# Kernel tuning notes

Hardware: AMD Instinct MI355X
Metric: run time of the kernel (lower is better)

The kernel has to match this reference:

```python
import jax, jax.numpy as jnp
import numpy as np

N_NODES = 20000
N_EDGES = 320000
N_GRAPHS = 64
SEQ = 20
SCALAR = 16
EMB = 32
HID = 128
HEADS = 4
IN_DIM = SCALAR + 5 * EMB  # 176
NEG_SLOPE = 0.2


def masked_mean_embed(table, idx):
    # table: [V, EMB], idx: [N, L] with 0 = padding
    emb = table[idx]                                  # [N, L, EMB]
    mask = (idx != 0).astype(emb.dtype)[..., None]    # [N, L, 1]
    return (emb * mask).sum(axis=1) / (mask.sum(axis=1) + 1e-9)


def gat_conv(x, src, dst, W, att_src, att_dst, bias, heads, out_ch):
    # PyG GATConv (add_self_loops already applied to src/dst), concat heads.
    N = x.shape[0]
    xw = (x @ W).reshape(N, heads, out_ch)            # [N, H, C]
    a_src = (xw * att_src).sum(-1)                    # [N, H]
    a_dst = (xw * att_dst).sum(-1)                    # [N, H]
    e = jax.nn.leaky_relu(a_src[src] + a_dst[dst], NEG_SLOPE)  # [E, H]
    e_max = jax.ops.segment_max(e, dst, num_segments=N)
    e_max = jnp.where(jnp.isfinite(e_max), e_max, 0.0)
    ex = jnp.exp(e - e_max[dst])                      # [E, H]
    denom = jax.ops.segment_sum(ex, dst, num_segments=N)
    alpha = ex / (denom[dst] + 1e-16)                 # [E, H]
    msg = xw[src] * alpha[:, :, None]                 # [E, H, C]
    out = jax.ops.segment_sum(msg, dst, num_segments=N)
    return out.reshape(N, heads * out_ch) + bias


def setup_inputs() -> dict:
    key = jax.random.key(0)
    ks = jax.random.split(key, 24)
    s = 0.05
    inp = {
        "x_scalar": jax.random.normal(ks[0], (N_NODES, SCALAR), jnp.float32),
        "x_opcode": jax.random.randint(ks[1], (N_NODES, SEQ), 0, 256),
        "x_source": jax.random.randint(ks[2], (N_NODES, SEQ), 0, 512),
        "x_sink": jax.random.randint(ks[3], (N_NODES, SEQ), 0, 512),
        "x_string_manip": jax.random.randint(ks[4], (N_NODES, SEQ), 0, 128),
        "x_payload": jax.random.randint(ks[5], (N_NODES, SEQ), 0, 1024),
        "edge_index": jax.random.randint(ks[6], (2, N_EDGES), 0, N_NODES),
        "batch": jnp.sort(jax.random.randint(ks[7], (N_NODES,), 0, N_GRAPHS)),
        # embedding tables (row 0 = padding; masked out anyway)
        "emb_opcode": jax.random.normal(ks[8], (256, EMB)) * s,
        "emb_source": jax.random.normal(ks[9], (512, EMB)) * s,
        "emb_sink": jax.random.normal(ks[10], (512, EMB)) * s,
        "emb_string": jax.random.normal(ks[11], (128, EMB)) * s,
        "emb_payload": jax.random.normal(ks[12], (1024, EMB)) * s,
        "ln_gamma": jnp.ones((IN_DIM,), jnp.float32),
        "ln_beta": jnp.zeros((IN_DIM,), jnp.float32),
        "W1": jax.random.normal(ks[13], (IN_DIM, HEADS * HID)) * s,
        "att_src1": jax.random.normal(ks[14], (HEADS, HID)) * s,
        "att_dst1": jax.random.normal(ks[15], (HEADS, HID)) * s,
        "b1": jnp.zeros((HEADS * HID,), jnp.float32),
        "W2": jax.random.normal(ks[16], (HEADS * HID, HID)) * s,
        "att_src2": jax.random.normal(ks[17], (1, HID)) * s,
        "att_dst2": jax.random.normal(ks[18], (1, HID)) * s,
        "b2": jnp.zeros((HID,), jnp.float32),
        "cls_w1": jax.random.normal(ks[19], (HID, HID // 2)) * s,
        "cls_b1": jnp.zeros((HID // 2,), jnp.float32),
        "cls_w2": jax.random.normal(ks[20], (HID // 2, 2)) * s,
        "cls_b2": jnp.zeros((2,), jnp.float32),
    }
    return inp


def reference(x_scalar, x_opcode, x_source, x_sink, x_string_manip, x_payload,
              edge_index, batch,
              emb_opcode, emb_source, emb_sink, emb_string, emb_payload,
              ln_gamma, ln_beta,
              W1, att_src1, att_dst1, b1,
              W2, att_src2, att_dst2, b2,
              cls_w1, cls_b1, cls_w2, cls_b2):
    feats = jnp.concatenate([
        x_scalar,
        masked_mean_embed(emb_opcode, x_opcode),
        masked_mean_embed(emb_source, x_source),
        masked_mean_embed(emb_sink, x_sink),
        masked_mean_embed(emb_string, x_string_manip),
        masked_mean_embed(emb_payload, x_payload),
    ], axis=1)  # [N, 176]
    mu = feats.mean(-1, keepdims=True)
    var = ((feats - mu) ** 2).mean(-1, keepdims=True)
    h = (feats - mu) / jnp.sqrt(var + 1e-5) * ln_gamma + ln_beta

    # add self loops (PyG GATConv default)
    loops = jnp.arange(N_NODES, dtype=edge_index.dtype)
    src = jnp.concatenate([edge_index[0], loops])
    dst = jnp.concatenate([edge_index[1], loops])

    x = jax.nn.elu(gat_conv(h, src, dst, W1, att_src1, att_dst1, b1, HEADS, HID))
    x = jax.nn.elu(gat_conv(x, src, dst, W2, att_src2, att_dst2, b2, 1, HID))

    pooled = jax.ops.segment_max(x, batch, num_segments=N_GRAPHS)  # [G, HID]
    hcls = jax.nn.relu(pooled @ cls_w1 + cls_b1)
    return hcls @ cls_w2 + cls_b2  # [G, 2]
```

## Files before the change

### kernel.cpp

```cpp
#include <hip/hip_runtime.h>
#include <hip/hip_bf16.h>
#include <math.h>

#define N_NODES 20000
#define N_EDGES 320000
#define N_GRAPHS 64
#define SEQ 20
#define SCALAR 16
#define EMB 32
#define HID 128
#define IN_DIM 176
#define TOT_EDGES (N_EDGES + N_NODES)
#define CHUNK_SMALL 10000
#define POOL_SLICES 32

typedef _Float16 half8v __attribute__((ext_vector_type(8)));
typedef float f32x4 __attribute__((ext_vector_type(4)));
#define LO_SCALE 2048.0f
#define LO_INV (1.0f / 2048.0f)

#define PB2_ELEMS (16 * 8 * 64 * 8)
#define PB1_ELEMS (4 * 6 * 8 * 64 * 8)

__device__ inline float readlane_f(float v, int l) {
  return __uint_as_float(__builtin_amdgcn_readlane(__float_as_uint(v), l));
}
__device__ inline int readlane_i(int v, int l) {
  return __builtin_amdgcn_readlane(v, l);
}
__device__ inline float leaky(float e) { return e >= 0.f ? e : 0.2f * e; }
__device__ inline float elu(float v) { return v > 0.f ? v : expf(v) - 1.f; }

__global__ __launch_bounds__(256) void feats_ln_kernel(
    const float* __restrict__ xs,
    const int* __restrict__ i0, const int* __restrict__ i1,
    const int* __restrict__ i2, const int* __restrict__ i3,
    const int* __restrict__ i4,
    const float* __restrict__ t0, const float* __restrict__ t1,
    const float* __restrict__ t2, const float* __restrict__ t3,
    const float* __restrict__ t4,
    const float* __restrict__ gamma, const float* __restrict__ beta,
    float* __restrict__ hout) {
  int lane = threadIdx.x & 63;
  int w = threadIdx.x >> 6;
  int n = blockIdx.x * 4 + w;
  if (n >= N_NODES) return;
  __shared__ int sidx[4][100];
  {
    int j = lane;
    int tab = j / 20, l = j - tab * 20;
    const int* ip = tab == 0 ? i0 : tab == 1 ? i1 : tab == 2 ? i2 : i3;
    sidx[w][j] = ip[n * SEQ + l];
    if (lane < 36) {
      int j2 = 64 + lane;
      int tab2 = j2 / 20, l2 = j2 - tab2 * 20;
      const int* ip2 = tab2 == 3 ? i3 : i4;
      sidx[w][j2] = ip2[n * SEQ + l2];
    }
  }
  bool l48 = lane < 48;
  float f0, f1, f2 = 0.f;
  if (lane < SCALAR) {
    f0 = xs[n * SCALAR + lane];
  } else {
    int tt = lane - SCALAR, tab = tt >> 5, d = tt & 31;
    const float* tp = tab == 0 ? t0 : t1;
    float sum = 0.f, cnt = 0.f;
#pragma unroll
    for (int l = 0; l < SEQ; ++l) {
      int id = sidx[w][tab * 20 + l];
      if (id != 0) { sum += tp[id * EMB + d]; cnt += 1.f; }
    }
    f0 = sum / (cnt + 1e-9f);
  }
  {
    int tt = 48 + lane, tab = tt >> 5, d = tt & 31;
    const float* tp = tab == 1 ? t1 : tab == 2 ? t2 : t3;
    float sum = 0.f, cnt = 0.f;
#pragma unroll
    for (int l = 0; l < SEQ; ++l) {
      int id = sidx[w][tab * 20 + l];
      if (id != 0) { sum += tp[id * EMB + d]; cnt += 1.f; }
    }
    f1 = sum / (cnt + 1e-9f);
  }
  if (l48) {
    int tt = 112 + lane, tab = tt >> 5, d = tt & 31;
    const float* tp = tab == 3 ? t3 : t4;
    float sum = 0.f, cnt = 0.f;
#pragma unroll
    for (int l = 0; l < SEQ; ++l) {
      int id = sidx[w][tab * 20 + l];
      if (id != 0) { sum += tp[id * EMB + d]; cnt += 1.f; }
    }
    f2 = sum / (cnt + 1e-9f);
  }
  float s = f0 + f1 + f2;
  for (int off = 1; off < 64; off <<= 1) s += __shfl_xor(s, off);
  float mu = s / (float)IN_DIM;
  float v = (f0 - mu) * (f0 - mu) + (f1 - mu) * (f1 - mu) +
            (l48 ? (f2 - mu) * (f2 - mu) : 0.f);
  for (int off = 1; off < 64; off <<= 1) v += __shfl_xor(v, off);
  float rstd = 1.0f / sqrtf(v / (float)IN_DIM + 1e-5f);
  float* hr = hout + (size_t)n * IN_DIM;
  hr[lane] = (f0 - mu) * rstd * gamma[lane] + beta[lane];
  hr[64 + lane] = (f1 - mu) * rstd * gamma[64 + lane] + beta[64 + lane];
  if (l48) hr[128 + lane] = (f2 - mu) * rstd * gamma[128 + lane] + beta[128 + lane];
}

__global__ void count_kernel(const int* __restrict__ edge_index,
                             int* __restrict__ cnt, int E, int N) {
  int i = blockIdx.x * blockDim.x + threadIdx.x;
  if (i < E) {
    atomicAdd(&cnt[edge_index[E + i]], 1);
  } else if (i < E + N) {
    atomicAdd(&cnt[i - E], 1);
  }
}

__global__ __launch_bounds__(256) void prefix_kernel(const int* __restrict__ cnt,
                                                     int* __restrict__ indptr,
                                                     int n, int total) {
  __shared__ int ssum[256];
  int t = threadIdx.x;
  int per = (n + 255) / 256;
  int beg = t * per, end = min(beg + per, n);
  int s = 0;
  for (int i = beg; i < end; ++i) s += cnt[i];
  ssum[t] = s;
  __syncthreads();
  if (t == 0) {
    int run = 0;
    for (int i = 0; i < 256; ++i) { int v = ssum[i]; ssum[i] = run; run += v; }
  }
  __syncthreads();
  int run = ssum[t];
  for (int i = beg; i < end; ++i) { indptr[i] = run; run += cnt[i]; }
  if (t == 0) indptr[n] = total;
}

__global__ void scatter_kernel(const int* __restrict__ edge_index,
                               const int* __restrict__ indptr,
                               int* __restrict__ cursor,
                               int* __restrict__ srcs, int E, int N) {
  int i = blockIdx.x * blockDim.x + threadIdx.x;
  int s, d;
  if (i < E) { s = edge_index[i]; d = edge_index[E + i]; }
  else if (i < E + N) { s = i - E; d = s; }
  else return;
  int pos = indptr[d] + atomicAdd(&cursor[d], 1);
  srcs[pos] = s;
}

__global__ __launch_bounds__(256) void wasd_kernel(
    const float* __restrict__ W1, const float* __restrict__ att_s,
    const float* __restrict__ att_d, float* __restrict__ was4,
    float* __restrict__ wad4) {
  int lane = threadIdx.x & 63;
  int k = blockIdx.x * 4 + (threadIdx.x >> 6);
  if (k >= IN_DIM) return;
  const float* wrow = W1 + (size_t)k * 512;
  float s[4], d[4];
#pragma unroll
  for (int hh = 0; hh < 4; ++hh) {
    float w0 = wrow[hh * 128 + lane], w1 = wrow[hh * 128 + 64 + lane];
    float a0 = att_s[hh * 128 + lane], a1 = att_s[hh * 128 + 64 + lane];
    float c0 = att_d[hh * 128 + lane], c1 = att_d[hh * 128 + 64 + lane];
    s[hh] = w0 * a0 + w1 * a1;
    d[hh] = w0 * c0 + w1 * c1;
  }
  for (int off = 1; off < 64; off <<= 1) {
#pragma unroll
    for (int hh = 0; hh < 4; ++hh) {
      s[hh] += __shfl_xor(s[hh], off);
      d[hh] += __shfl_xor(d[hh], off);
    }
  }
  if (lane == 0) {
    *(float4*)&was4[k * 4] = make_float4(s[0], s[1], s[2], s[3]);
    *(float4*)&wad4[k * 4] = make_float4(d[0], d[1], d[2], d[3]);
  }
}

__global__ __launch_bounds__(256) void att1h_kernel(
    const float* __restrict__ h, const float* __restrict__ was4,
    const float* __restrict__ wad4, float* __restrict__ a_s,
    float* __restrict__ a_d) {
  int lane = threadIdx.x & 63;
  int n = blockIdx.x * 4 + (threadIdx.x >> 6);
  if (n >= N_NODES) return;
  const float* hr = h + (size_t)n * IN_DIM;
  bool l48 = lane < 48;
  float v0 = hr[lane];
  float v1 = hr[64 + lane];
  float v2 = l48 ? hr[128 + lane] : 0.f;
  const float4* wsv = (const float4*)was4;
  const float4* wdv = (const float4*)wad4;
  float4 wsa = wsv[lane], wsb = wsv[64 + lane];
  float4 wsc = l48 ? wsv[128 + lane] : make_float4(0.f, 0.f, 0.f, 0.f);
  float4 wda = wdv[lane], wdb = wdv[64 + lane];
  float4 wdc = l48 ? wdv[128 + lane] : make_float4(0.f, 0.f, 0.f, 0.f);
  float ps0 = v0 * wsa.x + v1 * wsb.x + v2 * wsc.x;
  float ps1 = v0 * wsa.y + v1 * wsb.y + v2 * wsc.y;
  float ps2 = v0 * wsa.z + v1 * wsb.z + v2 * wsc.z;
  float ps3 = v0 * wsa.w + v1 * wsb.w + v2 * wsc.w;
  float pd0 = v0 * wda.x + v1 * wdb.x + v2 * wdc.x;
  float pd1 = v0 * wda.y + v1 * wdb.y + v2 * wdc.y;
  float pd2 = v0 * wda.z + v1 * wdb.z + v2 * wdc.z;
  float pd3 = v0 * wda.w + v1 * wdb.w + v2 * wdc.w;
  for (int off = 1; off < 64; off <<= 1) {
    ps0 += __shfl_xor(ps0, off); ps1 += __shfl_xor(ps1, off);
    ps2 += __shfl_xor(ps2, off); ps3 += __shfl_xor(ps3, off);
    pd0 += __shfl_xor(pd0, off); pd1 += __shfl_xor(pd1, off);
    pd2 += __shfl_xor(pd2, off); pd3 += __shfl_xor(pd3, off);
  }
  if (lane == 0) {
    *(float4*)&a_s[n * 4] = make_float4(ps0, ps1, ps2, ps3);
    *(float4*)&a_d[n * 4] = make_float4(pd0, pd1, pd2, pd3);
  }
}

__global__ __launch_bounds__(256) void agg1h_kernel(
    const float* __restrict__ h, const float* __restrict__ a_src,
    const float* __restrict__ a_dst, const int* __restrict__ indptr,
    const int* __restrict__ srcs, float* __restrict__ aggh,
    int n0, int nM) {
  int lane = threadIdx.x & 63;
  int ln = blockIdx.x * 4 + (threadIdx.x >> 6);
  if (ln >= nM) return;
  int n = n0 + ln;
  int beg = indptr[n], end = indptr[n + 1];
  int deg = end - beg;
  float4 ad = *(const float4*)&a_dst[n * 4];
  bool l48 = lane < 48;
  float acc[4][3] = {};

  auto body = [&](int s, float al0, float al1, float al2, float al3) {
    const float* r = h + (size_t)s * IN_DIM;
    float v0 = r[lane];
    float v1 = r[64 + lane];
    float v2 = l48 ? r[128 + lane] : 0.f;
    acc[0][0] += al0 * v0; acc[0][1] += al0 * v1; acc[0][2] += al0 * v2;
    acc[1][0] += al1 * v0; acc[1][1] += al1 * v1; acc[1][2] += al1 * v2;
    acc[2][0] += al2 * v0; acc[2][1] += al2 * v1; acc[2][2] += al2 * v2;
    acc[3][0] += al3 * v0; acc[3][1] += al3 * v1; acc[3][2] += al3 * v2;
  };

  if (deg <= 64) {
    int j = beg + lane;
    int s = 0;
    float e0 = -INFINITY, e1 = -INFINITY, e2 = -INFINITY, e3 = -INFINITY;
    if (j < end) {
      s = srcs[j];
      float4 as = *(const float4*)&a_src[s * 4];
      e0 = leaky(as.x + ad.x); e1 = leaky(as.y + ad.y);
      e2 = leaky(as.z + ad.z); e3 = leaky(as.w + ad.w);
    }
    float m0 = e0, m1 = e1, m2 = e2, m3 = e3;
    for (int off = 1; off < 64; off <<= 1) {
      m0 = fmaxf(m0, __shfl_xor(m0, off)); m1 = fmaxf(m1, __shfl_xor(m1, off));
      m2 = fmaxf(m2, __shfl_xor(m2, off)); m3 = fmaxf(m3, __shfl_xor(m3, off));
    }
    float x0 = (j < end) ? expf(e0 - m0) : 0.f;
    float x1 = (j < end) ? expf(e1 - m1) : 0.f;
    float x2 = (j < end) ? expf(e2 - m2) : 0.f;
    float x3 = (j < end) ? expf(e3 - m3) : 0.f;
    float d0 = x0, d1 = x1, d2 = x2, d3 = x3;
    for (int off = 1; off < 64; off <<= 1) {
      d0 += __shfl_xor(d0, off); d1 += __shfl_xor(d1, off);
      d2 += __shfl_xor(d2, off); d3 += __shfl_xor(d3, off);
    }
    float al0 = x0 / (d0 + 1e-16f), al1 = x1 / (d1 + 1e-16f);
    float al2 = x2 / (d2 + 1e-16f), al3 = x3 / (d3 + 1e-16f);
    int jj = 0;
    for (; jj + 2 <= deg; jj += 2) {
      int sa = readlane_i(s, jj), sb = readlane_i(s, jj + 1);
      float a0 = readlane_f(al0, jj), a1 = readlane_f(al1, jj);
      float a2 = readlane_f(al2, jj), a3 = readlane_f(al3, jj);
      float b0 = readlane_f(al0, jj + 1), b1 = readlane_f(al1, jj + 1);
      float b2 = readlane_f(al2, jj + 1), b3 = readlane_f(al3, jj + 1);
      body(sa, a0, a1, a2, a3);
      body(sb, b0, b1, b2, b3);
    }
    if (jj < deg) {
      int sa = readlane_i(s, jj);
      body(sa, readlane_f(al0, jj), readlane_f(al1, jj),
           readlane_f(al2, jj), readlane_f(al3, jj));
    }
  } else {
    float m0 = -INFINITY, m1 = -INFINITY, m2 = -INFINITY, m3 = -INFINITY;
    for (int j0 = beg; j0 < end; j0 += 64) {
      int j = j0 + lane;
      if (j < end) {
        int s = srcs[j];
        float4 as = *(const float4*)&a_src[s * 4];
        m0 = fmaxf(m0, leaky(as.x + ad.x)); m1 = fmaxf(m1, leaky(as.y + ad.y));
        m2 = fmaxf(m2, leaky(as.z + ad.z)); m3 = fmaxf(m3, leaky(as.w + ad.w));
      }
    }
    for (int off = 1; off < 64; off <<= 1) {
      m0 = fmaxf(m0, __shfl_xor(m0, off)); m1 = fmaxf(m1, __shfl_xor(m1, off));
      m2 = fmaxf(m2, __shfl_xor(m2, off)); m3 = fmaxf(m3, __shfl_xor(m3, off));
    }
    float d0 = 0.f, d1 = 0.f, d2 = 0.f, d3 = 0.f;
    for (int j0 = beg; j0 < end; j0 += 64) {
      int j = j0 + lane;
      if (j < end) {
        int s = srcs[j];
        float4 as = *(const float4*)&a_src[s * 4];
        d0 += expf(leaky(as.x + ad.x) - m0); d1 += expf(leaky(as.y + ad.y) - m1);
        d2 += expf(leaky(as.z + ad.z) - m2); d3 += expf(leaky(as.w + ad.w) - m3);
      }
    }
    for (int off = 1; off < 64; off <<= 1) {
      d0 += __shfl_xor(d0, off); d1 += __shfl_xor(d1, off);
      d2 += __shfl_xor(d2, off); d3 += __shfl_xor(d3, off);
    }
    float r0 = 1.f / (d0 + 1e-16f), r1 = 1.f / (d1 + 1e-16f);
    float r2 = 1.f / (d2 + 1e-16f), r3 = 1.f / (d3 + 1e-16f);
    for (int j0 = beg; j0 < end; j0 += 64) {
      int jn = min(64, end - j0);
      int j = j0 + lane;
      int s = 0;
      float al0 = 0.f, al1 = 0.f, al2 = 0.f, al3 = 0.f;
      if (j < end) {
        s = srcs[j];
        float4 as = *(const float4*)&a_src[s * 4];
        al0 = expf(leaky(as.x + ad.x) - m0) * r0;
        al1 = expf(leaky(as.y + ad.y) - m1) * r1;
        al2 = expf(leaky(as.z + ad.z) - m2) * r2;
        al3 = expf(leaky(as.w + ad.w) - m3) * r3;
      }
      for (int jj = 0; jj < jn; ++jj) {
        body(readlane_i(s, jj), readlane_f(al0, jj), readlane_f(al1, jj),
             readlane_f(al2, jj), readlane_f(al3, jj));
      }
    }
  }

  size_t base = (size_t)ln * (4 * IN_DIM);
#pragma unroll
  for (int hh = 0; hh < 4; ++hh) {
    aggh[base + hh * IN_DIM + lane] = acc[hh][0];
    aggh[base + hh * IN_DIM + 64 + lane] = acc[hh][1];
    if (l48) aggh[base + hh * IN_DIM + 128 + lane] = acc[hh][2];
  }
}

__global__ __launch_bounds__(256) void pack_w2_kernel(
    const float* __restrict__ W2, _Float16* __restrict__ PBh,
    _Float16* __restrict__ PBl) {
  int t = blockIdx.x * 256 + threadIdx.x;
  int lane = t & 63, wi = t >> 6;
  int r = lane & 15, g = lane >> 4;
  int ks = wi >> 3, ntile = wi & 7;
  int col = ntile * 16 + r;
  size_t o = ((size_t)wi * 64 + lane) * 8;
#pragma unroll
  for (int j = 0; j < 8; ++j) {
    int k = ks * 32 + g * 8 + j;
    float v = W2[(size_t)k * 128 + col];
    _Float16 h = (_Float16)v;
    PBh[o + j] = h;
    PBl[o + j] = (_Float16)((v - (float)h) * LO_SCALE);
  }
}

__global__ __launch_bounds__(256) void pack_w1_kernel(
    const float* __restrict__ W1, _Float16* __restrict__ PBh,
    _Float16* __restrict__ PBl) {
  int t = blockIdx.x * 256 + threadIdx.x;
  int lane = t & 63, wi = t >> 6;
  int r = lane & 15, g = lane >> 4;
  int ntile = wi & 7, rem = wi >> 3;
  int ks = rem % 6, hh = rem / 6;
  int col = hh * 128 + ntile * 16 + r;
  size_t o = ((size_t)wi * 64 + lane) * 8;
#pragma unroll
  for (int j = 0; j < 8; ++j) {
    int k = ks * 32 + g * 8 + j;
    float v = (k < IN_DIM) ? W1[(size_t)k * 512 + col] : 0.f;
    _Float16 h = (_Float16)v;
    PBh[o + j] = h;
    PBl[o + j] = (_Float16)((v - (float)h) * LO_SCALE);
  }
}

__global__ __launch_bounds__(256) void gemm_head_mfma_kernel(
    const float* __restrict__ aggh, const half8v* __restrict__ PBh,
    const half8v* __restrict__ PBl, const float* __restrict__ b1,
    float* __restrict__ out1, int M, int n0) {
  int lane = threadIdx.x & 63;
  int wid = (blockIdx.x * 256 + threadIdx.x) >> 6;
  int colhalf = wid & 1;
  int hh = (wid >> 1) & 3;
  int rg = wid >> 3;
  int rows0 = rg * 32;
  if (rows0 >= M) return;
  int r = lane & 15, g = lane >> 4;
  f32x4 acc[2][4] = {};
  f32x4 accm[2][4] = {};
  const float* a0 = aggh + ((size_t)(rows0 + r) * 4 + hh) * IN_DIM;
  const float* a1 = aggh + ((size_t)(rows0 + 16 + r) * 4 + hh) * IN_DIM;
#pragma unroll 2
  for (int ks = 0; ks < 6; ++ks) {
    int kg = ks * 32 + g * 8;
    int koff = (kg + 8 <= IN_DIM) ? kg : 0;
    half8v ah[2], al[2];
#pragma unroll
    for (int mt = 0; mt < 2; ++mt) {
      const float* ap = (mt ? a1 : a0) + koff;
      float av[8];
      *(float4*)&av[0] = *(const float4*)(ap);
      *(float4*)&av[4] = *(const float4*)(ap + 4);
#pragma unroll
      for (int j = 0; j < 8; ++j) {
        _Float16 hv = (_Float16)av[j];
        ah[mt][j] = hv;
        al[mt][j] = (_Float16)((av[j] - (float)hv) * LO_SCALE);
      }
    }
    const half8v* bh = PBh + (size_t)(((hh * 6 + ks) * 8 + colhalf * 4) * 64) + lane;
    const half8v* bl = PBl + (size_t)(((hh * 6 + ks) * 8 + colhalf * 4) * 64) + lane;
#pragma unroll
    for (int nt = 0; nt < 4; ++nt) {
      half8v bhv = bh[nt * 64], blv = bl[nt * 64];
#pragma unroll
      for (int mt = 0; mt < 2; ++mt) {
        accm[mt][nt] = __builtin_amdgcn_mfma_f32_16x16x32_f16(al[mt], bhv, accm[mt][nt], 0, 0, 0);
        accm[mt][nt] = __builtin_amdgcn_mfma_f32_16x16x32_f16(ah[mt], blv, accm[mt][nt], 0, 0, 0);
        acc[mt][nt]  = __builtin_amdgcn_mfma_f32_16x16x32_f16(ah[mt], bhv, acc[mt][nt], 0, 0, 0);
      }
    }
  }
#pragma unroll
  for (int nt = 0; nt < 4; ++nt) {
    int col = hh * 128 + colhalf * 64 + nt * 16 + r;
    float bb = b1[col];
#pragma unroll
    for (int mt = 0; mt < 2; ++mt) {
#pragma unroll
      for (int i = 0; i < 4; ++i) {
        int row = rows0 + mt * 16 + g * 4 + i;
        if (row < M)
          out1[(size_t)(n0 + row) * 512 + col] =
              elu(acc[mt][nt][i] + accm[mt][nt][i] * LO_INV + bb);
      }
    }
  }
}

__global__ __launch_bounds__(256) void gemm2att_mfma_kernel(
    const float* __restrict__ A, const half8v* __restrict__ PBh,
    const half8v* __restrict__ PBl, const float* __restrict__ att_s,
    const float* __restrict__ att_d, float* __restrict__ C,
    float* __restrict__ a_s, float* __restrict__ a_d, int M) {
  int lane = threadIdx.x & 63;
  int wid = (blockIdx.x * 256 + threadIdx.x) >> 6;
  int colhalf = wid & 1;
  int rg = wid >> 1;
  int row0 = rg * 16;
  if (row0 >= M) return;
  int r = lane & 15, g = lane >> 4;
  const float* arow = A + (size_t)(row0 + r) * 512 + g * 8;
  f32x4 acc[4] = {};
  f32x4 accm[4] = {};
#pragma unroll 2
  for (int ks = 0; ks < 16; ++ks) {
    float av[8];
    *(float4*)&av[0] = *(const float4*)(arow + ks * 32);
    *(float4*)&av[4] = *(const float4*)(arow + ks * 32 + 4);
    half8v ah, al;
#pragma unroll
    for (int j = 0; j < 8; ++j) {
      _Float16 hv = (_Float16)av[j];
      ah[j] = hv;
      al[j] = (_Float16)((av[j] - (float)hv) * LO_SCALE);
    }
    const half8v* bh = PBh + (size_t)((ks * 8 + colhalf * 4) * 64) + lane;
    const half8v* bl = PBl + (size_t)((ks * 8 + colhalf * 4) * 64) + lane;
#pragma unroll
    for (int nt = 0; nt < 4; ++nt) {
      half8v bhv = bh[nt * 64], blv = bl[nt * 64];
      accm[nt] = __builtin_amdgcn_mfma_f32_16x16x32_f16(al, bhv, accm[nt], 0, 0, 0);
      accm[nt] = __builtin_amdgcn_mfma_f32_16x16x32_f16(ah, blv, accm[nt], 0, 0, 0);
      acc[nt]  = __builtin_amdgcn_mfma_f32_16x16x32_f16(ah, bhv, acc[nt], 0, 0, 0);
    }
  }
  float ps[4] = {0.f, 0.f, 0.f, 0.f}, pd[4] = {0.f, 0.f, 0.f, 0.f};
#pragma unroll
  for (int nt = 0; nt < 4; ++nt) {
    int col = colhalf * 64 + nt * 16 + r;
    float as_ = att_s[col], ad_ = att_d[col];
#pragma unroll
    for (int i = 0; i < 4; ++i) {
      float v = acc[nt][i] + accm[nt][i] * LO_INV;
      int row = row0 + g * 4 + i;
      C[(size_t)row * 128 + col] = v;
      ps[i] += v * as_;
      pd[i] += v * ad_;
    }
  }
#pragma unroll
  for (int i = 0; i < 4; ++i) {
    for (int off = 1; off < 16; off <<= 1) {
      ps[i] += __shfl_xor(ps[i], off);
      pd[i] += __shfl_xor(pd[i], off);
    }
  }
  if (r == 0) {
#pragma unroll
    for (int i = 0; i < 4; ++i) {
      atomicAdd(&a_s[row0 + g * 4 + i], ps[i]);
      atomicAdd(&a_d[row0 + g * 4 + i], pd[i]);
    }
  }
}

__global__ __launch_bounds__(256) void agg2_kernel(
    const float* __restrict__ xw, const float* __restrict__ a_src,
    const float* __restrict__ a_dst, const int* __restrict__ indptr,
    const int* __restrict__ srcs, const float* __restrict__ bias,
    float* __restrict__ out) {
  int lane = threadIdx.x & 63;
  int n = blockIdx.x * 4 + (threadIdx.x >> 6);
  if (n >= N_NODES) return;
  int beg = indptr[n], end = indptr[n + 1];
  int deg = end - beg;
  float adn = a_dst[n];
  int half = lane >> 5, l32 = lane & 31;
  float4 acc = make_float4(0.f, 0.f, 0.f, 0.f);

  auto pairs = [&](int s, float al, int jn) {
    int jj = 0;
    for (; jj + 2 <= jn; jj += 2) {
      int sa = readlane_i(s, jj), sb = readlane_i(s, jj + 1);
      float aa = readlane_f(al, jj), ab = readlane_f(al, jj + 1);
      int sh = half ? sb : sa;
      float ahx = half ? ab : aa;
      float4 v = *(const float4*)&xw[(size_t)sh * HID + l32 * 4];
      acc.x += ahx * v.x; acc.y += ahx * v.y; acc.z += ahx * v.z; acc.w += ahx * v.w;
    }
    if (jj < jn) {
      int sa = readlane_i(s, jj);
      float ahx = half ? 0.f : readlane_f(al, jj);
      float4 v = *(const float4*)&xw[(size_t)sa * HID + l32 * 4];
      acc.x += ahx * v.x; acc.y += ahx * v.y; acc.z += ahx * v.z; acc.w += ahx * v.w;
    }
  };

  if (deg <= 64) {
    int j = beg + lane;
    int s = 0;
    float e = -INFINITY;
    if (j < end) { s = srcs[j]; e = leaky(a_src[s] + adn); }
    float m = e;
    for (int off = 1; off < 64; off <<= 1) m = fmaxf(m, __shfl_xor(m, off));
    float x = (j < end) ? expf(e - m) : 0.f;
    float d = x;
    for (int off = 1; off < 64; off <<= 1) d += __shfl_xor(d, off);
    float al = x / (d + 1e-16f);
    pairs(s, al, deg);
  } else {
    float m = -INFINITY;
    for (int j0 = beg; j0 < end; j0 += 64) {
      int j = j0 + lane;
      if (j < end) m = fmaxf(m, leaky(a_src[srcs[j]] + adn));
    }
    for (int off = 1; off < 64; off <<= 1) m = fmaxf(m, __shfl_xor(m, off));
    float d = 0.f;
    for (int j0 = beg; j0 < end; j0 += 64) {
      int j = j0 + lane;
      if (j < end) d += expf(leaky(a_src[srcs[j]] + adn) - m);
    }
    for (int off = 1; off < 64; off <<= 1) d += __shfl_xor(d, off);
    float rd = 1.f / (d + 1e-16f);
    for (int j0 = beg; j0 < end; j0 += 64) {
      int jn = min(64, end - j0);
      int j = j0 + lane;
      int s = 0;
      float al = 0.f;
      if (j < end) {
        s = srcs[j];
        al = expf(leaky(a_src[s] + adn) - m) * rd;
      }
      pairs(s, al, jn);
    }
  }

  acc.x += __shfl_xor(acc.x, 32); acc.y += __shfl_xor(acc.y, 32);
  acc.z += __shfl_xor(acc.z, 32); acc.w += __shfl_xor(acc.w, 32);
  if (half == 0) {
    float4 b = *(const float4*)&bias[l32 * 4];
    float4 o;
    o.x = elu(acc.x + b.x); o.y = elu(acc.y + b.y);
    o.z = elu(acc.z + b.z); o.w = elu(acc.w + b.w);
    *(float4*)&out[(size_t)n * HID + l32 * 4] = o;
  }
}

__global__ void gstart_kernel(const int* __restrict__ batch,
                              int* __restrict__ gstarts, int N, int G) {
  int t = threadIdx.x;
  if (t > G) return;
  int lo = 0, hi = N;
  while (lo < hi) {
    int mid = (lo + hi) >> 1;
    if (batch[mid] < t) lo = mid + 1; else hi = mid;
  }
  gstarts[t] = lo;
}

__global__ __launch_bounds__(HID) void pool_part_kernel(
    const float* __restrict__ out2, const int* __restrict__ gstarts,
    float* __restrict__ part) {
  int g = blockIdx.x, s = blockIdx.y, t = threadIdx.x;
  int beg = gstarts[g], end = gstarts[g + 1];
  int len = end - beg;
  int b0 = beg + (int)(((long long)len * s) / POOL_SLICES);
  int b1 = beg + (int)(((long long)len * (s + 1)) / POOL_SLICES);
  float m = -INFINITY;
  for (int n = b0; n < b1; ++n) m = fmaxf(m, out2[(size_t)n * HID + t]);
  part[((size_t)g * POOL_SLICES + s) * HID + t] = m;
}

__global__ __launch_bounds__(HID) void pool_reduce_kernel(
    const float* __restrict__ part, float* __restrict__ pooled) {
  int g = blockIdx.x, t = threadIdx.x;
  float m = -INFINITY;
#pragma unroll
  for (int s = 0; s < POOL_SLICES; ++s)
    m = fmaxf(m, part[((size_t)g * POOL_SLICES + s) * HID + t]);
  pooled[g * HID + t] = m;
}

__global__ __launch_bounds__(HID) void cls_kernel(const float* __restrict__ pooled,
                                                  const float* __restrict__ w1,
                                                  const float* __restrict__ b1,
                                                  const float* __restrict__ w2,
                                                  const float* __restrict__ b2,
                                                  float* __restrict__ out) {
  int g = blockIdx.x, t = threadIdx.x;
  __shared__ float sp[HID], sh1[HID / 2];
  sp[t] = pooled[g * HID + t];
  __syncthreads();
  if (t < HID / 2) {
    float s = b1[t];
    for (int k = 0; k < HID; ++k) s += sp[k] * w1[k * (HID / 2) + t];
    sh1[t] = fmaxf(s, 0.f);
  }
  __syncthreads();
  if (t < 2) {
    float o = b2[t];
    for (int k = 0; k < HID / 2; ++k) o += sh1[k] * w2[k * 2 + t];
    out[g * 2 + t] = o;
  }
}

extern "C" void kernel_launch(void* const* d_in, const int* in_sizes, int n_in,
                              void* d_out, int out_size, void* d_ws, size_t ws_size,
                              hipStream_t stream) {
  const float* x_scalar = (const float*)d_in[0];
  const int* x_opcode   = (const int*)d_in[1];
  const int* x_source   = (const int*)d_in[2];
  const int* x_sink     = (const int*)d_in[3];
  const int* x_string   = (const int*)d_in[4];
  const int* x_payload  = (const int*)d_in[5];
  const int* edge_index = (const int*)d_in[6];
  const int* batch      = (const int*)d_in[7];
  const float* emb_opcode = (const float*)d_in[8];
  const float* emb_source = (const float*)d_in[9];
  const float* emb_sink   = (const float*)d_in[10];
  const float* emb_string = (const float*)d_in[11];
  const float* emb_payload= (const float*)d_in[12];
  const float* ln_gamma = (const float*)d_in[13];
  const float* ln_beta  = (const float*)d_in[14];
  const float* W1       = (const float*)d_in[15];
  const float* att_src1 = (const float*)d_in[16];
  const float* att_dst1 = (const float*)d_in[17];
  const float* b1       = (const float*)d_in[18];
  const float* W2       = (const float*)d_in[19];
  const float* att_src2 = (const float*)d_in[20];
  const float* att_dst2 = (const float*)d_in[21];
  const float* b2       = (const float*)d_in[22];
  const float* cls_w1   = (const float*)d_in[23];
  const float* cls_b1   = (const float*)d_in[24];
  const float* cls_w2   = (const float*)d_in[25];
  const float* cls_b2   = (const float*)d_in[26];

  auto total_bytes = [&](int chunk) -> size_t {
    size_t f = (size_t)N_NODES * IN_DIM + (size_t)chunk * 4 * IN_DIM +
               (size_t)N_NODES * 512 + (size_t)N_NODES * HID +
               N_NODES * 4 * 2 + N_NODES * 2 + IN_DIM * 4 * 2 + N_GRAPHS * HID;
    size_t ii = (N_NODES + 1) + N_NODES * 2 + TOT_EDGES + (N_GRAPHS + 1);
    size_t f16b = (size_t)2 * (PB2_ELEMS + PB1_ELEMS) * sizeof(_Float16) + 32;
    size_t poolb = (size_t)N_GRAPHS * POOL_SLICES * HID * 4 + 32;
    return f * 4 + ii * 4 + f16b + poolb + 256;
  };
  int chunk = (ws_size >= total_bytes(N_NODES)) ? N_NODES : CHUNK_SMALL;

  float* h      = (float*)d_ws;
  float* aggh   = h + (size_t)N_NODES * IN_DIM;
  float* out1   = aggh + (size_t)chunk * 4 * IN_DIM;
  float* out2   = out1 + (size_t)N_NODES * 512;
  float* a1s    = out2 + (size_t)N_NODES * HID;
  float* a1d    = a1s + N_NODES * 4;
  float* was4   = a1d + N_NODES * 4;
  float* wad4   = was4 + IN_DIM * 4;
  float* pooled = wad4 + IN_DIM * 4;
  int* indptr = (int*)(pooled + N_GRAPHS * HID);
  int* cnt    = indptr + (N_NODES + 1);
  int* cursor = cnt + N_NODES;
  float* a2s  = (float*)(cursor + N_NODES);
  float* a2d  = a2s + N_NODES;
  int* srcs   = (int*)(a2d + N_NODES);
  int* gstarts= srcs + TOT_EDGES;
  uintptr_t pal = ((uintptr_t)(gstarts + N_GRAPHS + 1) + 15) & ~(uintptr_t)15;
  _Float16* PB2h = (_Float16*)pal;
  _Float16* PB2l = PB2h + PB2_ELEMS;
  _Float16* PB1h = PB2l + PB2_ELEMS;
  _Float16* PB1l = PB1h + PB1_ELEMS;
  uintptr_t ppal = ((uintptr_t)(PB1l + PB1_ELEMS) + 15) & ~(uintptr_t)15;
  float* pool_part = (float*)ppal;
  float* xw2  = h;

  hipMemsetAsync(cnt, 0, 4 * N_NODES * sizeof(int), stream);

  const int NB4 = (N_NODES + 3) / 4;
  feats_ln_kernel<<<NB4, 256, 0, stream>>>(
      x_scalar, x_opcode, x_source, x_sink, x_string, x_payload,
      emb_opcode, emb_source, emb_sink, emb_string, emb_payload,
      ln_gamma, ln_beta, h);

  int nthreads = TOT_EDGES;
  count_kernel<<<(nthreads + 255) / 256, 256, 0, stream>>>(edge_index, cnt, N_EDGES, N_NODES);
  prefix_kernel<<<1, 256, 0, stream>>>(cnt, indptr, N_NODES, TOT_EDGES);
  scatter_kernel<<<(nthreads + 255) / 256, 256, 0, stream>>>(edge_index, indptr, cursor, srcs, N_EDGES, N_NODES);

  wasd_kernel<<<(IN_DIM + 3) / 4, 256, 0, stream>>>(W1, att_src1, att_dst1, was4, wad4);
  pack_w1_kernel<<<48, 256, 0, stream>>>(W1, PB1h, PB1l);
  pack_w2_kernel<<<32, 256, 0, stream>>>(W2, PB2h, PB2l);

  att1h_kernel<<<NB4, 256, 0, stream>>>(h, was4, wad4, a1s, a1d);

  for (int n0 = 0; n0 < N_NODES; n0 += chunk) {
    int nM = min(chunk, N_NODES - n0);
    agg1h_kernel<<<(nM + 3) / 4, 256, 0, stream>>>(h, a1s, a1d, indptr, srcs, aggh, n0, nM);
    int rgs = (nM + 31) / 32;
    gemm_head_mfma_kernel<<<rgs * 2, 256, 0, stream>>>(
        aggh, (const half8v*)PB1h, (const half8v*)PB1l, b1, out1, nM, n0);
  }

  gemm2att_mfma_kernel<<<((N_NODES + 15) / 16 * 2 + 3) / 4, 256, 0, stream>>>(
      out1, (const half8v*)PB2h, (const half8v*)PB2l, att_src2, att_dst2,
      xw2, a2s, a2d, N_NODES);

  agg2_kernel<<<NB4, 256, 0, stream>>>(xw2, a2s, a2d, indptr, srcs, b2, out2);

  gstart_kernel<<<1, 128, 0, stream>>>(batch, gstarts, N_NODES, N_GRAPHS);
  pool_part_kernel<<<dim3(N_GRAPHS, POOL_SLICES), HID, 0, stream>>>(out2, gstarts, pool_part);
  pool_reduce_kernel<<<N_GRAPHS, HID, 0, stream>>>(pool_part, pooled);
  cls_kernel<<<N_GRAPHS, HID, 0, stream>>>(pooled, cls_w1, cls_b1, cls_w2, cls_b2, (float*)d_out);
}
```

Baseline: 403.0 us.

## Reorder GAT layer 1 to transform before aggregating and fuse layer-2 GEMM per chunk

Layer 1 now runs the 176→512 GEMM on node features first, with attention logits computed in the GEMM epilogue. Edges then gather 512-wide transformed rows per head, replacing the old scheme that aggregated 176-wide raw features per head into a 4×176 buffer and ran the GEMM afterwards. The layer-2 GEMM is moved into the per-chunk loop so out1 lives in a chunk-sized buffer. This trades edge-gather bytes (512 floats per edge instead of 176) for a smaller GEMM and lower intermediate traffic, and it adds atomics for the layer-1 attention logits.

Result: slower. 437.0 us (+8.4%).

```diff
diff --git a/kernel.cpp b/kernel.cpp
--- a/kernel.cpp
+++ b/kernel.cpp
@@ -152,79 +152,132 @@
   srcs[pos] = s;
 }
 
-__global__ __launch_bounds__(256) void wasd_kernel(
-    const float* __restrict__ W1, const float* __restrict__ att_s,
-    const float* __restrict__ att_d, float* __restrict__ was4,
-    float* __restrict__ wad4) {
+__global__ __launch_bounds__(256) void pack_w2_kernel(
+    const float* __restrict__ W2, _Float16* __restrict__ PBh,
+    _Float16* __restrict__ PBl) {
+  int t = blockIdx.x * 256 + threadIdx.x;
+  int lane = t & 63, wi = t >> 6;
+  int r = lane & 15, g = lane >> 4;
+  int ks = wi >> 3, ntile = wi & 7;
+  int col = ntile * 16 + r;
+  size_t o = ((size_t)wi * 64 + lane) * 8;
+#pragma unroll
+  for (int j = 0; j < 8; ++j) {
+    int k = ks * 32 + g * 8 + j;
+    float v = W2[(size_t)k * 128 + col];
+    _Float16 h = (_Float16)v;
+    PBh[o + j] = h;
+    PBl[o + j] = (_Float16)((v - (float)h) * LO_SCALE);
+  }
+}
+
+__global__ __launch_bounds__(256) void pack_w1_kernel(
+    const float* __restrict__ W1, _Float16* __restrict__ PBh,
+    _Float16* __restrict__ PBl) {
+  int t = blockIdx.x * 256 + threadIdx.x;
+  int lane = t & 63, wi = t >> 6;
+  int r = lane & 15, g = lane >> 4;
+  int ntile = wi & 7, rem = wi >> 3;
+  int ks = rem % 6, hh = rem / 6;
+  int col = hh * 128 + ntile * 16 + r;
+  size_t o = ((size_t)wi * 64 + lane) * 8;
+#pragma unroll
+  for (int j = 0; j < 8; ++j) {
+    int k = ks * 32 + g * 8 + j;
+    float v = (k < IN_DIM) ? W1[(size_t)k * 512 + col] : 0.f;
+    _Float16 h = (_Float16)v;
+    PBh[o + j] = h;
+    PBl[o + j] = (_Float16)((v - (float)h) * LO_SCALE);
+  }
+}
+
+__global__ __launch_bounds__(256) void gemm1_mfma_kernel(
+    const float* __restrict__ h, const half8v* __restrict__ PBh,
+    const half8v* __restrict__ PBl, const float* __restrict__ att_s,
+    const float* __restrict__ att_d, float* __restrict__ hw,
+    float* __restrict__ a_s, float* __restrict__ a_d, int M) {
   int lane = threadIdx.x & 63;
-  int k = blockIdx.x * 4 + (threadIdx.x >> 6);
-  if (k >= IN_DIM) return;
-  const float* wrow = W1 + (size_t)k * 512;
-  float s[4], d[4];
-#pragma unroll
-  for (int hh = 0; hh < 4; ++hh) {
-    float w0 = wrow[hh * 128 + lane], w1 = wrow[hh * 128 + 64 + lane];
-    float a0 = att_s[hh * 128 + lane], a1 = att_s[hh * 128 + 64 + lane];
-    float c0 = att_d[hh * 128 + lane], c1 = att_d[hh * 128 + 64 + lane];
-    s[hh] = w0 * a0 + w1 * a1;
-    d[hh] = w0 * c0 + w1 * c1;
-  }
-  for (int off = 1; off < 64; off <<= 1) {
-#pragma unroll
-    for (int hh = 0; hh < 4; ++hh) {
-      s[hh] += __shfl_xor(s[hh], off);
-      d[hh] += __shfl_xor(d[hh], off);
-    }
-  }
-  if (lane == 0) {
-    *(float4*)&was4[k * 4] = make_float4(s[0], s[1], s[2], s[3]);
-    *(float4*)&wad4[k * 4] = make_float4(d[0], d[1], d[2], d[3]);
-  }
-}
-
-__global__ __launch_bounds__(256) void att1h_kernel(
-    const float* __restrict__ h, const float* __restrict__ was4,
-    const float* __restrict__ wad4, float* __restrict__ a_s,
-    float* __restrict__ a_d) {
-  int lane = threadIdx.x & 63;
-  int n = blockIdx.x * 4 + (threadIdx.x >> 6);
-  if (n >= N_NODES) return;
-  const float* hr = h + (size_t)n * IN_DIM;
-  bool l48 = lane < 48;
-  float v0 = hr[lane];
-  float v1 = hr[64 + lane];
-  float v2 = l48 ? hr[128 + lane] : 0.f;
-  const float4* wsv = (const float4*)was4;
-  const float4* wdv = (const float4*)wad4;
-  float4 wsa = wsv[lane], wsb = wsv[64 + lane];
-  float4 wsc = l48 ? wsv[128 + lane] : make_float4(0.f, 0.f, 0.f, 0.f);
-  float4 wda = wdv[lane], wdb = wdv[64 + lane];
-  float4 wdc = l48 ? wdv[128 + lane] : make_float4(0.f, 0.f, 0.f, 0.f);
-  float ps0 = v0 * wsa.x + v1 * wsb.x + v2 * wsc.x;
-  float ps1 = v0 * wsa.y + v1 * wsb.y + v2 * wsc.y;
-  float ps2 = v0 * wsa.z + v1 * wsb.z + v2 * wsc.z;
-  float ps3 = v0 * wsa.w + v1 * wsb.w + v2 * wsc.w;
-  float pd0 = v0 * wda.x + v1 * wdb.x + v2 * wdc.x;
-  float pd1 = v0 * wda.y + v1 * wdb.y + v2 * wdc.y;
-  float pd2 = v0 * wda.z + v1 * wdb.z + v2 * wdc.z;
-  float pd3 = v0 * wda.w + v1 * wdb.w + v2 * wdc.w;
-  for (int off = 1; off < 64; off <<= 1) {
-    ps0 += __shfl_xor(ps0, off); ps1 += __shfl_xor(ps1, off);
-    ps2 += __shfl_xor(ps2, off); ps3 += __shfl_xor(ps3, off);
-    pd0 += __shfl_xor(pd0, off); pd1 += __shfl_xor(pd1, off);
-    pd2 += __shfl_xor(pd2, off); pd3 += __shfl_xor(pd3, off);
-  }
-  if (lane == 0) {
-    *(float4*)&a_s[n * 4] = make_float4(ps0, ps1, ps2, ps3);
-    *(float4*)&a_d[n * 4] = make_float4(pd0, pd1, pd2, pd3);
-  }
-}
-
-__global__ __launch_bounds__(256) void agg1h_kernel(
-    const float* __restrict__ h, const float* __restrict__ a_src,
+  int wid = (blockIdx.x * 256 + threadIdx.x) >> 6;
+  int colhalf = wid & 1;
+  int hh = (wid >> 1) & 3;
+  int rg = wid >> 3;
+  int rows0 = rg * 32;
+  if (rows0 >= M) return;
+  int r = lane & 15, g = lane >> 4;
+  f32x4 acc[2][4] = {};
+  f32x4 accm[2][4] = {};
+  const float* a0 = h + (size_t)(rows0 + r) * IN_DIM;
+  const float* a1 = h + (size_t)(rows0 + 16 + r) * IN_DIM;
+#pragma unroll 2
+  for (int ks = 0; ks < 6; ++ks) {
+    int kg = ks * 32 + g * 8;
+    int koff = (kg + 8 <= IN_DIM) ? kg : 0;
+    half8v ah[2], al[2];
+#pragma unroll
+    for (int mt = 0; mt < 2; ++mt) {
+      const float* ap = (mt ? a1 : a0) + koff;
+      float av[8];
+      *(float4*)&av[0] = *(const float4*)(ap);
+      *(float4*)&av[4] = *(const float4*)(ap + 4);
+#pragma unroll
+      for (int j = 0; j < 8; ++j) {
+        _Float16 hv = (_Float16)av[j];
+        ah[mt][j] = hv;
+        al[mt][j] = (_Float16)((av[j] - (float)hv) * LO_SCALE);
+      }
+    }
+    const half8v* bh = PBh + (size_t)(((hh * 6 + ks) * 8 + colhalf * 4) * 64) + lane;
+    const half8v* bl = PBl + (size_t)(((hh * 6 + ks) * 8 + colhalf * 4) * 64) + lane;
+#pragma unroll
+    for (int nt = 0; nt < 4; ++nt) {
+      half8v bhv = bh[nt * 64], blv = bl[nt * 64];
+#pragma unroll
+      for (int mt = 0; mt < 2; ++mt) {
+        accm[mt][nt] = __builtin_amdgcn_mfma_f32_16x16x32_f16(al[mt], bhv, accm[mt][nt], 0, 0, 0);
+        accm[mt][nt] = __builtin_amdgcn_mfma_f32_16x16x32_f16(ah[mt], blv, accm[mt][nt], 0, 0, 0);
+        acc[mt][nt]  = __builtin_amdgcn_mfma_f32_16x16x32_f16(ah[mt], bhv, acc[mt][nt], 0, 0, 0);
+      }
+    }
+  }
+  float ps[2][4] = {}, pd[2][4] = {};
+#pragma unroll
+  for (int nt = 0; nt < 4; ++nt) {
+    int col = hh * 128 + colhalf * 64 + nt * 16 + r;
+    float as_ = att_s[col], ad_ = att_d[col];
+#pragma unroll
+    for (int mt = 0; mt < 2; ++mt) {
+#pragma unroll
+      for (int i = 0; i < 4; ++i) {
+        float v = acc[mt][nt][i] + accm[mt][nt][i] * LO_INV;
+        int row = rows0 + mt * 16 + g * 4 + i;
+        if (row < M) hw[(size_t)row * 512 + col] = v;
+        ps[mt][i] += v * as_;
+        pd[mt][i] += v * ad_;
+      }
+    }
+  }
+#pragma unroll
+  for (int mt = 0; mt < 2; ++mt) {
+#pragma unroll
+    for (int i = 0; i < 4; ++i) {
+      for (int off = 1; off < 16; off <<= 1) {
+        ps[mt][i] += __shfl_xor(ps[mt][i], off);
+        pd[mt][i] += __shfl_xor(pd[mt][i], off);
+      }
+      int row = rows0 + mt * 16 + g * 4 + i;
+      if (r == 0 && row < M) {
+        atomicAdd(&a_s[row * 4 + hh], ps[mt][i]);
+        atomicAdd(&a_d[row * 4 + hh], pd[mt][i]);
+      }
+    }
+  }
+}
+
+__global__ __launch_bounds__(256) void agg1_kernel(
+    const float* __restrict__ hw, const float* __restrict__ a_src,
     const float* __restrict__ a_dst, const int* __restrict__ indptr,
-    const int* __restrict__ srcs, float* __restrict__ aggh,
-    int n0, int nM) {
+    const int* __restrict__ srcs, const float* __restrict__ bias,
+    float* __restrict__ out1, int n0, int nM) {
   int lane = threadIdx.x & 63;
   int ln = blockIdx.x * 4 + (threadIdx.x >> 6);
   if (ln >= nM) return;
@@ -232,18 +285,19 @@
   int beg = indptr[n], end = indptr[n + 1];
   int deg = end - beg;
   float4 ad = *(const float4*)&a_dst[n * 4];
-  bool l48 = lane < 48;
-  float acc[4][3] = {};
-
-  auto body = [&](int s, float al0, float al1, float al2, float al3) {
-    const float* r = h + (size_t)s * IN_DIM;
-    float v0 = r[lane];
-    float v1 = r[64 + lane];
-    float v2 = l48 ? r[128 + lane] : 0.f;
-    acc[0][0] += al0 * v0; acc[0][1] += al0 * v1; acc[0][2] += al0 * v2;
-    acc[1][0] += al1 * v0; acc[1][1] += al1 * v1; acc[1][2] += al1 * v2;
-    acc[2][0] += al2 * v0; acc[2][1] += al2 * v1; acc[2][2] += al2 * v2;
-    acc[3][0] += al3 * v0; acc[3][1] += al3 * v1; acc[3][2] += al3 * v2;
+  int hd = lane >> 4;
+  float4 acc0 = make_float4(0.f, 0.f, 0.f, 0.f);
+  float4 acc1 = make_float4(0.f, 0.f, 0.f, 0.f);
+
+  auto body = [&](int s, float a) {
+    const float* rp = hw + (size_t)s * 512 + lane * 8;
+    float4 v0 = *(const float4*)rp;
+    float4 v1 = *(const float4*)(rp + 4);
+    acc0.x += a * v0.x; acc0.y += a * v0.y; acc0.z += a * v0.z; acc0.w += a * v0.w;
+    acc1.x += a * v1.x; acc1.y += a * v1.y; acc1.z += a * v1.z; acc1.w += a * v1.w;
+  };
+  auto pick = [&](float q0, float q1, float q2, float q3) {
+    return hd == 0 ? q0 : hd == 1 ? q1 : hd == 2 ? q2 : q3;
   };
 
   if (deg <= 64) {
@@ -275,17 +329,18 @@
     int jj = 0;
     for (; jj + 2 <= deg; jj += 2) {
       int sa = readlane_i(s, jj), sb = readlane_i(s, jj + 1);
-      float a0 = readlane_f(al0, jj), a1 = readlane_f(al1, jj);
-      float a2 = readlane_f(al2, jj), a3 = readlane_f(al3, jj);
-      float b0 = readlane_f(al0, jj + 1), b1 = readlane_f(al1, jj + 1);
-      float b2 = readlane_f(al2, jj + 1), b3 = readlane_f(al3, jj + 1);
-      body(sa, a0, a1, a2, a3);
-      body(sb, b0, b1, b2, b3);
+      float aa = pick(readlane_f(al0, jj), readlane_f(al1, jj),
+                      readlane_f(al2, jj), readlane_f(al3, jj));
+      float ab = pick(readlane_f(al0, jj + 1), readlane_f(al1, jj + 1),
+                      readlane_f(al2, jj + 1), readlane_f(al3, jj + 1));
+      body(sa, aa);
+      body(sb, ab);
     }
     if (jj < deg) {
       int sa = readlane_i(s, jj);
-      body(sa, readlane_f(al0, jj), readlane_f(al1, jj),
-           readlane_f(al2, jj), readlane_f(al3, jj));
+      float aa = pick(readlane_f(al0, jj), readlane_f(al1, jj),
+                      readlane_f(al2, jj), readlane_f(al3, jj));
+      body(sa, aa);
     }
   } else {
     float m0 = -INFINITY, m1 = -INFINITY, m2 = -INFINITY, m3 = -INFINITY;
@@ -332,135 +387,38 @@
         al3 = expf(leaky(as.w + ad.w) - m3) * r3;
       }
       for (int jj = 0; jj < jn; ++jj) {
-        body(readlane_i(s, jj), readlane_f(al0, jj), readlane_f(al1, jj),
-             readlane_f(al2, jj), readlane_f(al3, jj));
-      }
-    }
-  }
-
-  size_t base = (size_t)ln * (4 * IN_DIM);
-#pragma unroll
-  for (int hh = 0; hh < 4; ++hh) {
-    aggh[base + hh * IN_DIM + lane] = acc[hh][0];
-    aggh[base + hh * IN_DIM + 64 + lane] = acc[hh][1];
-    if (l48) aggh[base + hh * IN_DIM + 128 + lane] = acc[hh][2];
-  }
-}
-
-__global__ __launch_bounds__(256) void pack_w2_kernel(
-    const float* __restrict__ W2, _Float16* __restrict__ PBh,
-    _Float16* __restrict__ PBl) {
-  int t = blockIdx.x * 256 + threadIdx.x;
-  int lane = t & 63, wi = t >> 6;
-  int r = lane & 15, g = lane >> 4;
-  int ks = wi >> 3, ntile = wi & 7;
-  int col = ntile * 16 + r;
-  size_t o = ((size_t)wi * 64 + lane) * 8;
-#pragma unroll
-  for (int j = 0; j < 8; ++j) {
-    int k = ks * 32 + g * 8 + j;
-    float v = W2[(size_t)k * 128 + col];
-    _Float16 h = (_Float16)v;
-    PBh[o + j] = h;
-    PBl[o + j] = (_Float16)((v - (float)h) * LO_SCALE);
-  }
-}
-
-__global__ __launch_bounds__(256) void pack_w1_kernel(
-    const float* __restrict__ W1, _Float16* __restrict__ PBh,
-    _Float16* __restrict__ PBl) {
-  int t = blockIdx.x * 256 + threadIdx.x;
-  int lane = t & 63, wi = t >> 6;
-  int r = lane & 15, g = lane >> 4;
-  int ntile = wi & 7, rem = wi >> 3;
-  int ks = rem % 6, hh = rem / 6;
-  int col = hh * 128 + ntile * 16 + r;
-  size_t o = ((size_t)wi * 64 + lane) * 8;
-#pragma unroll
-  for (int j = 0; j < 8; ++j) {
-    int k = ks * 32 + g * 8 + j;
-    float v = (k < IN_DIM) ? W1[(size_t)k * 512 + col] : 0.f;
-    _Float16 h = (_Float16)v;
-    PBh[o + j] = h;
-    PBl[o + j] = (_Float16)((v - (float)h) * LO_SCALE);
-  }
-}
-
-__global__ __launch_bounds__(256) void gemm_head_mfma_kernel(
-    const float* __restrict__ aggh, const half8v* __restrict__ PBh,
-    const half8v* __restrict__ PBl, const float* __restrict__ b1,
-    float* __restrict__ out1, int M, int n0) {
-  int lane = threadIdx.x & 63;
-  int wid = (blockIdx.x * 256 + threadIdx.x) >> 6;
-  int colhalf = wid & 1;
-  int hh = (wid >> 1) & 3;
-  int rg = wid >> 3;
-  int rows0 = rg * 32;
-  if (rows0 >= M) return;
-  int r = lane & 15, g = lane >> 4;
-  f32x4 acc[2][4] = {};
-  f32x4 accm[2][4] = {};
-  const float* a0 = aggh + ((size_t)(rows0 + r) * 4 + hh) * IN_DIM;
-  const float* a1 = aggh + ((size_t)(rows0 + 16 + r) * 4 + hh) * IN_DIM;
-#pragma unroll 2
-  for (int ks = 0; ks < 6; ++ks) {
-    int kg = ks * 32 + g * 8;
-    int koff = (kg + 8 <= IN_DIM) ? kg : 0;
-    half8v ah[2], al[2];
-#pragma unroll
-    for (int mt = 0; mt < 2; ++mt) {
-      const float* ap = (mt ? a1 : a0) + koff;
-      float av[8];
-      *(float4*)&av[0] = *(const float4*)(ap);
-      *(float4*)&av[4] = *(const float4*)(ap + 4);
-#pragma unroll
-      for (int j = 0; j < 8; ++j) {
-        _Float16 hv = (_Float16)av[j];
-        ah[mt][j] = hv;
-        al[mt][j] = (_Float16)((av[j] - (float)hv) * LO_SCALE);
-      }
-    }
-    const half8v* bh = PBh + (size_t)(((hh * 6 + ks) * 8 + colhalf * 4) * 64) + lane;
-    const half8v* bl = PBl + (size_t)(((hh * 6 + ks) * 8 + colhalf * 4) * 64) + lane;
-#pragma unroll
-    for (int nt = 0; nt < 4; ++nt) {
-      half8v bhv = bh[nt * 64], blv = bl[nt * 64];
-#pragma unroll
-      for (int mt = 0; mt < 2; ++mt) {
-        accm[mt][nt] = __builtin_amdgcn_mfma_f32_16x16x32_f16(al[mt], bhv, accm[mt][nt], 0, 0, 0);
-        accm[mt][nt] = __builtin_amdgcn_mfma_f32_16x16x32_f16(ah[mt], blv, accm[mt][nt], 0, 0, 0);
-        acc[mt][nt]  = __builtin_amdgcn_mfma_f32_16x16x32_f16(ah[mt], bhv, acc[mt][nt], 0, 0, 0);
-      }
-    }
-  }
-#pragma unroll
-  for (int nt = 0; nt < 4; ++nt) {
-    int col = hh * 128 + colhalf * 64 + nt * 16 + r;
-    float bb = b1[col];
-#pragma unroll
-    for (int mt = 0; mt < 2; ++mt) {
-#pragma unroll
-      for (int i = 0; i < 4; ++i) {
-        int row = rows0 + mt * 16 + g * 4 + i;
-        if (row < M)
-          out1[(size_t)(n0 + row) * 512 + col] =
-              elu(acc[mt][nt][i] + accm[mt][nt][i] * LO_INV + bb);
-      }
-    }
-  }
+        int sa = readlane_i(s, jj);
+        float aa = pick(readlane_f(al0, jj), readlane_f(al1, jj),
+                        readlane_f(al2, jj), readlane_f(al3, jj));
+        body(sa, aa);
+      }
+    }
+  }
+
+  const float* bp = bias + lane * 8;
+  float4 b0 = *(const float4*)bp;
+  float4 b1v = *(const float4*)(bp + 4);
+  float4 o0, o1;
+  o0.x = elu(acc0.x + b0.x); o0.y = elu(acc0.y + b0.y);
+  o0.z = elu(acc0.z + b0.z); o0.w = elu(acc0.w + b0.w);
+  o1.x = elu(acc1.x + b1v.x); o1.y = elu(acc1.y + b1v.y);
+  o1.z = elu(acc1.z + b1v.z); o1.w = elu(acc1.w + b1v.w);
+  size_t ob = (size_t)ln * 512 + lane * 8;
+  *(float4*)&out1[ob] = o0;
+  *(float4*)&out1[ob + 4] = o1;
 }
 
 __global__ __launch_bounds__(256) void gemm2att_mfma_kernel(
     const float* __restrict__ A, const half8v* __restrict__ PBh,
     const half8v* __restrict__ PBl, const float* __restrict__ att_s,
     const float* __restrict__ att_d, float* __restrict__ C,
-    float* __restrict__ a_s, float* __restrict__ a_d, int M) {
+    float* __restrict__ a_s, float* __restrict__ a_d, int nM, int n0) {
   int lane = threadIdx.x & 63;
   int wid = (blockIdx.x * 256 + threadIdx.x) >> 6;
   int colhalf = wid & 1;
   int rg = wid >> 1;
   int row0 = rg * 16;
-  if (row0 >= M) return;
+  if (row0 >= nM) return;
   int r = lane & 15, g = lane >> 4;
   const float* arow = A + (size_t)(row0 + r) * 512 + g * 8;
   f32x4 acc[4] = {};
@@ -496,7 +454,7 @@
     for (int i = 0; i < 4; ++i) {
       float v = acc[nt][i] + accm[nt][i] * LO_INV;
       int row = row0 + g * 4 + i;
-      C[(size_t)row * 128 + col] = v;
+      if (row < nM) C[(size_t)(n0 + row) * 128 + col] = v;
       ps[i] += v * as_;
       pd[i] += v * ad_;
     }
@@ -511,8 +469,11 @@
   if (r == 0) {
 #pragma unroll
     for (int i = 0; i < 4; ++i) {
-      atomicAdd(&a_s[row0 + g * 4 + i], ps[i]);
-      atomicAdd(&a_d[row0 + g * 4 + i], pd[i]);
+      int row = row0 + g * 4 + i;
+      if (row < nM) {
+        atomicAdd(&a_s[n0 + row], ps[i]);
+        atomicAdd(&a_d[n0 + row], pd[i]);
+      }
     }
   }
 }
@@ -689,42 +650,42 @@
   const float* cls_b2   = (const float*)d_in[26];
 
   auto total_bytes = [&](int chunk) -> size_t {
-    size_t f = (size_t)N_NODES * IN_DIM + (size_t)chunk * 4 * IN_DIM +
-               (size_t)N_NODES * 512 + (size_t)N_NODES * HID +
-               N_NODES * 4 * 2 + N_NODES * 2 + IN_DIM * 4 * 2 + N_GRAPHS * HID;
-    size_t ii = (N_NODES + 1) + N_NODES * 2 + TOT_EDGES + (N_GRAPHS + 1);
-    size_t f16b = (size_t)2 * (PB2_ELEMS + PB1_ELEMS) * sizeof(_Float16) + 32;
-    size_t poolb = (size_t)N_GRAPHS * POOL_SLICES * HID * 4 + 32;
-    return f * 4 + ii * 4 + f16b + poolb + 256;
+    size_t f32w = (size_t)N_NODES * IN_DIM
+                + (size_t)N_NODES * 512
+                + (size_t)chunk * 512
+                + (size_t)N_NODES * HID
+                + (size_t)N_GRAPHS * HID
+                + (size_t)N_GRAPHS * POOL_SLICES * HID;
+    size_t ints = (N_NODES + 1) + 12 * (size_t)N_NODES + TOT_EDGES + (N_GRAPHS + 1);
+    size_t f16e = 2 * (size_t)(PB2_ELEMS + PB1_ELEMS);
+    return f32w * 4 + ints * 4 + f16e * 2 + 512;
   };
   int chunk = (ws_size >= total_bytes(N_NODES)) ? N_NODES : CHUNK_SMALL;
 
   float* h      = (float*)d_ws;
-  float* aggh   = h + (size_t)N_NODES * IN_DIM;
-  float* out1   = aggh + (size_t)chunk * 4 * IN_DIM;
-  float* out2   = out1 + (size_t)N_NODES * 512;
-  float* a1s    = out2 + (size_t)N_NODES * HID;
-  float* a1d    = a1s + N_NODES * 4;
-  float* was4   = a1d + N_NODES * 4;
-  float* wad4   = was4 + IN_DIM * 4;
-  float* pooled = wad4 + IN_DIM * 4;
-  int* indptr = (int*)(pooled + N_GRAPHS * HID);
+  float* hw     = h + (size_t)N_NODES * IN_DIM;
+  float* out2   = hw + (size_t)N_NODES * 512;
+  float* pooled = out2 + (size_t)N_NODES * HID;
+  float* pool_part = pooled + N_GRAPHS * HID;
+  int* indptr = (int*)(pool_part + (size_t)N_GRAPHS * POOL_SLICES * HID);
   int* cnt    = indptr + (N_NODES + 1);
   int* cursor = cnt + N_NODES;
   float* a2s  = (float*)(cursor + N_NODES);
   float* a2d  = a2s + N_NODES;
-  int* srcs   = (int*)(a2d + N_NODES);
+  float* a1s  = a2d + N_NODES;
+  float* a1d  = a1s + (size_t)N_NODES * 4;
+  int* srcs   = (int*)(a1d + (size_t)N_NODES * 4);
   int* gstarts= srcs + TOT_EDGES;
   uintptr_t pal = ((uintptr_t)(gstarts + N_GRAPHS + 1) + 15) & ~(uintptr_t)15;
   _Float16* PB2h = (_Float16*)pal;
   _Float16* PB2l = PB2h + PB2_ELEMS;
   _Float16* PB1h = PB2l + PB2_ELEMS;
   _Float16* PB1l = PB1h + PB1_ELEMS;
-  uintptr_t ppal = ((uintptr_t)(PB1l + PB1_ELEMS) + 15) & ~(uintptr_t)15;
-  float* pool_part = (float*)ppal;
-  float* xw2  = h;
-
-  hipMemsetAsync(cnt, 0, 4 * N_NODES * sizeof(int), stream);
+  uintptr_t oal = ((uintptr_t)(PB1l + PB1_ELEMS) + 15) & ~(uintptr_t)15;
+  float* out1c = (float*)oal;
+  float* xw2 = h;
+
+  hipMemsetAsync(cnt, 0, 12 * (size_t)N_NODES * sizeof(int), stream);
 
   const int NB4 = (N_NODES + 3) / 4;
   feats_ln_kernel<<<NB4, 256, 0, stream>>>(
@@ -737,23 +698,22 @@
   prefix_kernel<<<1, 256, 0, stream>>>(cnt, indptr, N_NODES, TOT_EDGES);
   scatter_kernel<<<(nthreads + 255) / 256, 256, 0, stream>>>(edge_index, indptr, cursor, srcs, N_EDGES, N_NODES);
 
-  wasd_kernel<<<(IN_DIM + 3) / 4, 256, 0, stream>>>(W1, att_src1, att_dst1, was4, wad4);
   pack_w1_kernel<<<48, 256, 0, stream>>>(W1, PB1h, PB1l);
   pack_w2_kernel<<<32, 256, 0, stream>>>(W2, PB2h, PB2l);
 
-  att1h_kernel<<<NB4, 256, 0, stream>>>(h, was4, wad4, a1s, a1d);
+  int rgs1 = (N_NODES + 31) / 32;
+  gemm1_mfma_kernel<<<rgs1 * 2, 256, 0, stream>>>(
+      h, (const half8v*)PB1h, (const half8v*)PB1l, att_src1, att_dst1,
+      hw, a1s, a1d, N_NODES);
 
   for (int n0 = 0; n0 < N_NODES; n0 += chunk) {
     int nM = min(chunk, N_NODES - n0);
-    agg1h_kernel<<<(nM + 3) / 4, 256, 0, stream>>>(h, a1s, a1d, indptr, srcs, aggh, n0, nM);
-    int rgs = (nM + 31) / 32;
-    gemm_head_mfma_kernel<<<rgs * 2, 256, 0, stream>>>(
-        aggh, (const half8v*)PB1h, (const half8v*)PB1l, b1, out1, nM, n0);
-  }
-
-  gemm2att_mfma_kernel<<<((N_NODES + 15) / 16 * 2 + 3) / 4, 256, 0, stream>>>(
-      out1, (const half8v*)PB2h, (const half8v*)PB2l, att_src2, att_dst2,
-      xw2, a2s, a2d, N_NODES);
+    agg1_kernel<<<(nM + 3) / 4, 256, 0, stream>>>(
+        hw, a1s, a1d, indptr, srcs, b1, out1c, n0, nM);
+    gemm2att_mfma_kernel<<<((nM + 15) / 16 * 2 + 3) / 4, 256, 0, stream>>>(
+        out1c, (const half8v*)PB2h, (const half8v*)PB2l, att_src2, att_dst2,
+        xw2, a2s, a2d, nM, n0);
+  }
 
   agg2_kernel<<<NB4, 256, 0, stream>>>(xw2, a2s, a2d, indptr, srcs, b2, out2);
 
```
